# Kernel tuning notes

Measured on AMD Instinct MI355X. Metric: run time of the kernel, lower is better.

## Reference

```python
import jax, jax.numpy as jnp
import numpy as np
import math

HIDDEN = 128   # hidden_size (per-head dim) used for 1/sqrt(d) scaling
SPAN = 1024    # attn_span
B, M = 32, 1024
K_LEN = M + SPAN


def _unskew(X, span):
    """X: [B, M, K] -> [B, M, span], out[b,m,l] = X[b, m, m+l].
    Equivalent to the torch pad/view/slice trick (shift row m left by m)."""
    _, Mq, _ = X.shape
    rows = jnp.arange(Mq)[:, None]                 # [M,1]
    cols = rows + jnp.arange(span)[None, :]        # [M,span]
    return X[:, rows, cols]


def _skew(X, pad_value):
    """X: [B, M, L] -> [B, M, M+L], out[b,m,j] = X[b,m,j-m] if 0<=j-m<L else pad.
    Equivalent to the torch pad/view/slice trick (shift row m right by m)."""
    _, Mq, L = X.shape
    m = jnp.arange(Mq)[:, None]                    # [M,1]
    rel = jnp.arange(Mq + L)[None, :] - m          # [M, M+L]
    valid = (rel >= 0) & (rel < L)
    gathered = X[:, m, jnp.clip(rel, 0, L - 1)]    # [B, M, M+L]
    return jnp.where(valid, gathered, pad_value)


def setup_inputs() -> dict:
    key = jax.random.key(0)
    k1, k2, k3, k4 = jax.random.split(key, 4)
    return {
        "query": jax.random.normal(k1, (B, M, HIDDEN), dtype=jnp.float32),
        "key": jax.random.normal(k2, (B, K_LEN, HIDDEN), dtype=jnp.float32),
        "value": jax.random.normal(k3, (B, K_LEN, HIDDEN), dtype=jnp.float32),
        "pos_encoding": jax.random.normal(k4, (HIDDEN, SPAN), dtype=jnp.float32),
    }


def reference(query, key, value, pos_encoding):
    span = pos_encoding.shape[-1]
    # context scores: [B, M, M+span]
    attn_ctx = jnp.einsum('bmh,bkh->bmk', query, key)
    attn_ctx = _unskew(attn_ctx, span)             # [B, M, span]
    # relative-position scores: [B, M, span]
    attn_pos = jnp.einsum('bmh,hl->bml', query, pos_encoding)
    attn = (attn_ctx + attn_pos) / math.sqrt(HIDDEN)
    attn = jax.nn.softmax(attn, axis=-1)           # dropout p=0 -> identity
    attn_sk = _skew(attn, 0.0)                     # [B, M, M+span]
    return jnp.einsum('bmk,bkh->bmh', attn_sk, value)
```

## Files before the change

kernel.cpp:

```cpp
#include <hip/hip_runtime.h>
#include <hip/hip_bf16.h>

#define B_    32
#define M_    1024
#define H_    128
#define SPAN_ 1024
#define KL_   2048
#define NITER 17

typedef __attribute__((ext_vector_type(8))) short bf16x8;
typedef __attribute__((ext_vector_type(4))) float f32x4;

#define PITCH_A  264
#define PITCH_VT 136
#define PITCH_PR 264
#define PITCH_PW 136
#define OFF_K  0
#define OFF_VT 16896
#define OFF_PT 34304
#define OFF_PR 51200
#define OFF_PW 68096
#define LDS_TOTAL 76800
#define SCALE 0.08838834764831845f

static __device__ __forceinline__ unsigned int cvt_pk2(float lo, float hi) {
  unsigned int r;
  asm("v_cvt_pk_bf16_f32 %0, %1, %2" : "=v"(r) : "v"(lo), "v"(hi));
  return r;
}
static __device__ __forceinline__ unsigned short f2b(float x) {
  unsigned int u = __builtin_bit_cast(unsigned int, x);
  return (unsigned short)((u + 0x7FFFu + ((u >> 16) & 1u)) >> 16);
}
static __device__ __forceinline__ float b2f(unsigned short u) {
  return __builtin_bit_cast(float, ((unsigned int)u) << 16);
}
static __device__ __forceinline__ bf16x8 ldfrag(const char* p) {
  short4 a = *(const short4*)p;
  short4 b = *(const short4*)(p + 8);
  bf16x8 r;
  r[0] = a.x; r[1] = a.y; r[2] = a.z; r[3] = a.w;
  r[4] = b.x; r[5] = b.y; r[6] = b.z; r[7] = b.w;
  return r;
}

__global__ void __launch_bounds__(256, 2) seqattn_kernel(
    const float* __restrict__ q, const float* __restrict__ kkey,
    const float* __restrict__ vval, const float* __restrict__ pe,
    float* __restrict__ out) {
  extern __shared__ char smem[];
  char* KL = smem + OFF_K;
  char* VT = smem + OFF_VT;
  char* PT = smem + OFF_PT;
  char* PR = smem + OFF_PR;
  char* PW = smem + OFF_PW;

  int jb = blockIdx.x;
  int o  = (jb & 7) * 64 + (jb >> 3);
  int b  = o >> 4;
  int m0 = (o & 15) * 64;

  int tid  = threadIdx.x;
  int w    = tid >> 6;
  int lane = tid & 63;
  int g    = lane >> 4;
  int c    = lane & 15;
  int r0   = tid >> 5;
  int c4   = tid & 31;

  const float* qbase = q    + ((size_t)b * M_  + m0) * H_;
  const float* kbase = kkey + ((size_t)b * KL_ + m0) * H_;
  const float* vbase = vval + ((size_t)b * KL_ + m0) * H_;

  float4 kpre[8];
  float  vpre[32];
  float  ppre[32];

#define LOADK(tt) do {                                                        \
    const float* kb_ = kbase + (size_t)(64 * (tt)) * H_;                      \
    _Pragma("unroll")                                                         \
    for (int p = 0; p < 8; ++p)                                               \
      kpre[p] = *(const float4*)(kb_ + (p * 8 + r0) * H_ + c4 * 4);           \
  } while (0)

#define WRITEK() do {                                                         \
    _Pragma("unroll")                                                         \
    for (int p = 0; p < 8; ++p) {                                             \
      float4 v_ = kpre[p];                                                    \
      uint2 d_; d_.x = cvt_pk2(v_.x, v_.y); d_.y = cvt_pk2(v_.z, v_.w);       \
      *(uint2*)(KL + (p * 8 + r0) * PITCH_A + c4 * 8) = d_;                   \
    }                                                                         \
  } while (0)

#define LOADV(tt) do {                                                        \
    const float* vb_ = vbase + (size_t)(64 * (tt)) * H_;                      \
    _Pragma("unroll")                                                         \
    for (int qq = 0; qq < 4; ++qq) {                                          \
      int kq_ = 4 * (4 * w + qq);                                             \
      _Pragma("unroll")                                                       \
      for (int r = 0; r < 4; ++r) {                                           \
        vpre[qq * 8 + r * 2 + 0] = vb_[(kq_ + r) * H_ + lane];                \
        vpre[qq * 8 + r * 2 + 1] = vb_[(kq_ + r) * H_ + lane + 64];           \
      }                                                                       \
    }                                                                         \
  } while (0)

#define WRITEV() do {                                                         \
    _Pragma("unroll")                                                         \
    for (int qq = 0; qq < 4; ++qq) {                                          \
      int kq_ = 4 * w + qq;                                                   \
      uint2 lo_, hi_;                                                         \
      lo_.x = cvt_pk2(vpre[qq * 8 + 0], vpre[qq * 8 + 2]);                    \
      lo_.y = cvt_pk2(vpre[qq * 8 + 4], vpre[qq * 8 + 6]);                    \
      hi_.x = cvt_pk2(vpre[qq * 8 + 1], vpre[qq * 8 + 3]);                    \
      hi_.y = cvt_pk2(vpre[qq * 8 + 5], vpre[qq * 8 + 7]);                    \
      *(uint2*)(VT + lane * PITCH_VT + 8 * kq_) = lo_;                        \
      *(uint2*)(VT + (lane + 64) * PITCH_VT + 8 * kq_) = hi_;                 \
    }                                                                         \
  } while (0)

#define LOADP(tt) do {                                                        \
    const float* pb_ = pe + 64 * (tt);                                        \
    _Pragma("unroll")                                                         \
    for (int qq = 0; qq < 8; ++qq) {                                          \
      int h_ = 4 * (8 * w + qq);                                              \
      _Pragma("unroll")                                                       \
      for (int r = 0; r < 4; ++r)                                             \
        ppre[qq * 4 + r] = pb_[(h_ + r) * SPAN_ + lane];                      \
    }                                                                         \
  } while (0)

#define WRITEP() do {                                                         \
    _Pragma("unroll")                                                         \
    for (int qq = 0; qq < 8; ++qq) {                                          \
      uint2 d_;                                                               \
      d_.x = cvt_pk2(ppre[qq * 4 + 0], ppre[qq * 4 + 1]);                     \
      d_.y = cvt_pk2(ppre[qq * 4 + 2], ppre[qq * 4 + 3]);                     \
      *(uint2*)(PT + lane * PITCH_A + 8 * (8 * w + qq)) = d_;                 \
    }                                                                         \
  } while (0)

  {
    float4 qpre[8];
#pragma unroll
    for (int p = 0; p < 8; ++p)
      qpre[p] = *(const float4*)(qbase + (p * 8 + r0) * H_ + c4 * 4);
    LOADK(0); LOADV(0); LOADP(0);
#pragma unroll
    for (int p = 0; p < 8; ++p) {
      float4 v_ = qpre[p];
      uint2 d_;
      d_.x = cvt_pk2(v_.x * SCALE, v_.y * SCALE);
      d_.y = cvt_pk2(v_.z * SCALE, v_.w * SCALE);
      *(uint2*)(PR + (p * 8 + r0) * PITCH_PR + c4 * 8) = d_;
    }
    WRITEK(); WRITEV(); WRITEP();
    LOADK(1); LOADV(1); LOADP(1);
  }
  __syncthreads();

  bf16x8 qf[4];
#pragma unroll
  for (int hs = 0; hs < 4; ++hs)
    qf[hs] = ldfrag(PR + (w * 16 + c) * PITCH_PR + hs * 64 + g * 16);

  f32x4 O[8];
#pragma unroll
  for (int i = 0; i < 8; ++i) { O[i][0] = 0.f; O[i][1] = 0.f; O[i][2] = 0.f; O[i][3] = 0.f; }
  float mrun = -1e30f, lrun = 0.f;
  const int mrow = 16 * w + c;
  char* prRow = PR + mrow * PITCH_PR;
  char* pwRow = PW + mrow * PITCH_PW;

#pragma unroll 1
  for (int t = 0; t < NITER; ++t) {
    if (t < 16) {
#pragma unroll
      for (int lt = 0; lt < 4; ++lt) {
        f32x4 pb = {0.f, 0.f, 0.f, 0.f};
#pragma unroll
        for (int hs = 0; hs < 4; ++hs)
          pb = __builtin_amdgcn_mfma_f32_16x16x32_bf16(
              ldfrag(PT + (16 * lt + c) * PITCH_A + hs * 64 + g * 16), qf[hs], pb, 0, 0, 0);
#pragma unroll
        for (int rr = 0; rr < 4; ++rr) {
          int x = (64 * t + 16 * lt + 4 * g + rr + mrow) & 127;
          *(unsigned short*)(prRow + x * 2) = f2b(pb[rr]);
        }
      }
    }

    f32x4 s[4];
#pragma unroll
    for (int nt = 0; nt < 4; ++nt) {
      f32x4 acc = {0.f, 0.f, 0.f, 0.f};
#pragma unroll
      for (int hs = 0; hs < 4; ++hs)
        acc = __builtin_amdgcn_mfma_f32_16x16x32_bf16(
            ldfrag(KL + (16 * nt + c) * PITCH_A + hs * 64 + g * 16), qf[hs], acc, 0, 0, 0);
      s[nt] = acc;
    }

#pragma unroll
    for (int nt = 0; nt < 4; ++nt) {
      int x = (64 * t + 16 * nt + 4 * g) & 127;
      ushort4 bv = *(const ushort4*)(prRow + x * 2);
      int lbase = 64 * t + 16 * nt + 4 * g - mrow;
      const unsigned short* bp = (const unsigned short*)&bv;
#pragma unroll
      for (int rr = 0; rr < 4; ++rr) {
        float sv = s[nt][rr] + b2f(bp[rr]);
        s[nt][rr] = ((unsigned)(lbase + rr) < 1024u) ? sv : -1e30f;
      }
    }

    float pmax = -1e30f;
#pragma unroll
    for (int nt = 0; nt < 4; ++nt)
#pragma unroll
      for (int rr = 0; rr < 4; ++rr) pmax = fmaxf(pmax, s[nt][rr]);
    pmax = fmaxf(pmax, __shfl_xor(pmax, 16, 64));
    pmax = fmaxf(pmax, __shfl_xor(pmax, 32, 64));

    if (__any(pmax > mrun + 8.0f)) {
      float mn = fmaxf(mrun, pmax);
      float corr = __expf(mrun - mn);
      mrun = mn;
      lrun *= corr;
#pragma unroll
      for (int i = 0; i < 8; ++i) {
        O[i][0] *= corr; O[i][1] *= corr; O[i][2] *= corr; O[i][3] *= corr;
      }
    }

    float rsum = 0.f;
#pragma unroll
    for (int nt = 0; nt < 4; ++nt) {
      float p0 = __expf(s[nt][0] - mrun);
      float p1 = __expf(s[nt][1] - mrun);
      float p2 = __expf(s[nt][2] - mrun);
      float p3 = __expf(s[nt][3] - mrun);
      rsum += (p0 + p1) + (p2 + p3);
      uint2 d_;
      d_.x = cvt_pk2(p0, p1);
      d_.y = cvt_pk2(p2, p3);
      *(uint2*)(pwRow + (16 * nt + 4 * g) * 2) = d_;
    }
    rsum += __shfl_xor(rsum, 16, 64);
    rsum += __shfl_xor(rsum, 32, 64);
    lrun += rsum;

#pragma unroll
    for (int ks = 0; ks < 2; ++ks) {
      bf16x8 pfrag = ldfrag(pwRow + ks * 64 + g * 16);
#pragma unroll
      for (int nt = 0; nt < 8; ++nt)
        O[nt] = __builtin_amdgcn_mfma_f32_16x16x32_bf16(
            ldfrag(VT + (16 * nt + c) * PITCH_VT + ks * 64 + g * 16), pfrag, O[nt], 0, 0, 0);
    }

    __syncthreads();
    if (t < 16) {
      WRITEK(); WRITEV();
      if (t < 15) {
        WRITEP();
        LOADK(t + 2); LOADV(t + 2);
        if (t + 2 < 16) LOADP(t + 2);
      }
    }
    __syncthreads();
  }

  float inv = 1.0f / lrun;
  float* ob = out + ((size_t)b * M_ + m0 + mrow) * H_;
#pragma unroll
  for (int nt = 0; nt < 8; ++nt) {
    float4 vv;
    vv.x = O[nt][0] * inv; vv.y = O[nt][1] * inv;
    vv.z = O[nt][2] * inv; vv.w = O[nt][3] * inv;
    *(float4*)(ob + 16 * nt + 4 * g) = vv;
  }
}

extern "C" void kernel_launch(void* const* d_in, const int* in_sizes, int n_in,
                              void* d_out, int out_size, void* d_ws, size_t ws_size,
                              hipStream_t stream) {
  const float* q  = (const float*)d_in[0];
  const float* k  = (const float*)d_in[1];
  const float* v  = (const float*)d_in[2];
  const float* pe = (const float*)d_in[3];
  float* out = (float*)d_out;

  hipFuncSetAttribute(reinterpret_cast<const void*>(seqattn_kernel),
                      hipFuncAttributeMaxDynamicSharedMemorySize, LDS_TOTAL);
  seqattn_kernel<<<dim3(512), dim3(256), LDS_TOTAL, stream>>>(q, k, v, pe, out);
}
```

Before: 79.07 us.

## Pre-convert Q/K/V/pos to swizzled bf16 in workspace and stream via global_load_lds

Adds four pre-pass kernels that convert query (pre-scaled), key, transposed value and transposed pos_encoding to bf16 in a workspace, laid out in an XOR-swizzled tile layout. The main attention kernel then loads these tiles directly into LDS with global_load_lds, with no register staging or conversion in the loop, and hoists V fragments into registers so the next tile's prefetch can be issued earlier. This cuts fp32 global traffic and per-iteration conversion work inside the main loop. The cost is extra launches and a full extra read/write pass over the inputs. The old kernel stays as a fallback when the workspace is too small.

```diff
diff --git a/kernel.cpp b/kernel.cpp
--- a/kernel.cpp
+++ b/kernel.cpp
@@ -7,9 +7,289 @@
 #define SPAN_ 1024
 #define KL_   2048
 #define NITER 17
+#define SCALE 0.08838834764831845f
 
 typedef __attribute__((ext_vector_type(8))) short bf16x8;
 typedef __attribute__((ext_vector_type(4))) float f32x4;
+
+#define QOFF 0ull
+#define KOFF 8388608ull
+#define VOFF 25165824ull
+#define POFF 41943040ull
+#define WSNEED 42205184ull
+
+static __device__ __forceinline__ unsigned int cvt_pk2(float lo, float hi) {
+  unsigned int r;
+  asm("v_cvt_pk_bf16_f32 %0, %1, %2" : "=v"(r) : "v"(lo), "v"(hi));
+  return r;
+}
+static __device__ __forceinline__ unsigned short f2b(float x) {
+  unsigned int u = __builtin_bit_cast(unsigned int, x);
+  return (unsigned short)((u + 0x7FFFu + ((u >> 16) & 1u)) >> 16);
+}
+static __device__ __forceinline__ float b2f(unsigned short u) {
+  return __builtin_bit_cast(float, ((unsigned int)u) << 16);
+}
+static __device__ __forceinline__ bf16x8 ldfrag(const char* p) {
+  short4 a = *(const short4*)p;
+  short4 b = *(const short4*)(p + 8);
+  bf16x8 r;
+  r[0] = a.x; r[1] = a.y; r[2] = a.z; r[3] = a.w;
+  r[4] = b.x; r[5] = b.y; r[6] = b.z; r[7] = b.w;
+  return r;
+}
+static __device__ __forceinline__ void gll16(char* lds, const char* g) {
+  __builtin_amdgcn_global_load_lds(
+      (const __attribute__((address_space(1))) unsigned int*)g,
+      (__attribute__((address_space(3))) unsigned int*)lds, 16, 0, 0);
+}
+
+__global__ void convA(const float* __restrict__ in, char* __restrict__ out,
+                      int nunits, float scale) {
+  int idx = blockIdx.x * 256 + threadIdx.x;
+  if (idx >= nunits) return;
+  int r = idx >> 4, u = idx & 15;
+  const float* p = in + (size_t)r * 128 + u * 8;
+  float4 a = *(const float4*)p, b = *(const float4*)(p + 4);
+  uint4 d;
+  d.x = cvt_pk2(a.x * scale, a.y * scale);
+  d.y = cvt_pk2(a.z * scale, a.w * scale);
+  d.z = cvt_pk2(b.x * scale, b.y * scale);
+  d.w = cvt_pk2(b.z * scale, b.w * scale);
+  *(uint4*)(out + (size_t)r * 256 + 16 * (u ^ (r & 7))) = d;
+}
+
+__global__ void convV(const float* __restrict__ v, char* __restrict__ out) {
+  __shared__ float tile[64][130];
+  int tb = blockIdx.x;
+  const float* src = v + (size_t)tb * 64 * 128;
+  int tid = threadIdx.x;
+#pragma unroll
+  for (int i = 0; i < 8; ++i) {
+    int idx = i * 256 + tid;
+    int row = idx >> 5, c4 = idx & 31;
+    float4 x = *(const float4*)(src + row * 128 + c4 * 4);
+    tile[row][c4 * 4 + 0] = x.x; tile[row][c4 * 4 + 1] = x.y;
+    tile[row][c4 * 4 + 2] = x.z; tile[row][c4 * 4 + 3] = x.w;
+  }
+  __syncthreads();
+  char* dst = out + (size_t)tb * 16384;
+#pragma unroll
+  for (int j = 0; j < 4; ++j) {
+    int idx = j * 256 + tid;
+    int h = idx >> 3, u = idx & 7;
+    uint4 d;
+    d.x = cvt_pk2(tile[8 * u + 0][h], tile[8 * u + 1][h]);
+    d.y = cvt_pk2(tile[8 * u + 2][h], tile[8 * u + 3][h]);
+    d.z = cvt_pk2(tile[8 * u + 4][h], tile[8 * u + 5][h]);
+    d.w = cvt_pk2(tile[8 * u + 6][h], tile[8 * u + 7][h]);
+    *(uint4*)(dst + h * 128 + 16 * (u ^ (h & 7))) = d;
+  }
+}
+
+__global__ void convP(const float* __restrict__ pe, char* __restrict__ out) {
+  __shared__ float tile[128][66];
+  int lt = blockIdx.x, tid = threadIdx.x;
+#pragma unroll
+  for (int i = 0; i < 8; ++i) {
+    int idx = i * 256 + tid;
+    int h = idx >> 4, c4 = idx & 15;
+    float4 x = *(const float4*)(pe + (size_t)h * 1024 + lt * 64 + c4 * 4);
+    tile[h][c4 * 4 + 0] = x.x; tile[h][c4 * 4 + 1] = x.y;
+    tile[h][c4 * 4 + 2] = x.z; tile[h][c4 * 4 + 3] = x.w;
+  }
+  __syncthreads();
+  char* dst = out + (size_t)lt * 16384;
+#pragma unroll
+  for (int j = 0; j < 4; ++j) {
+    int idx = j * 256 + tid;
+    int l = idx >> 4, u = idx & 15;
+    uint4 d;
+    d.x = cvt_pk2(tile[8 * u + 0][l], tile[8 * u + 1][l]);
+    d.y = cvt_pk2(tile[8 * u + 2][l], tile[8 * u + 3][l]);
+    d.z = cvt_pk2(tile[8 * u + 4][l], tile[8 * u + 5][l]);
+    d.w = cvt_pk2(tile[8 * u + 6][l], tile[8 * u + 7][l]);
+    *(uint4*)(dst + l * 256 + 16 * (u ^ (l & 7))) = d;
+  }
+}
+
+#define L_KL 0
+#define L_VT 16384
+#define L_PT 32768
+#define L_PR 49152
+#define L_PW 66048
+#define LDS_MAIN 74752
+
+__global__ void __launch_bounds__(256, 2) seqattn_main(
+    const char* __restrict__ qws, const char* __restrict__ kws,
+    const char* __restrict__ vws, const char* __restrict__ pws,
+    float* __restrict__ out) {
+  extern __shared__ char smem[];
+  char* KL = smem + L_KL;
+  char* VT = smem + L_VT;
+  char* PT = smem + L_PT;
+  char* PR = smem + L_PR;
+  char* PW = smem + L_PW;
+
+  int jb = blockIdx.x;
+  int o  = (jb & 7) * 64 + (jb >> 3);
+  int b  = o >> 4;
+  int m0t = o & 15;
+
+  int tid = threadIdx.x, w = tid >> 6, lane = tid & 63, g = lane >> 4, c = lane & 15;
+  int mrow = 16 * w + c;
+  int sx = c & 7;
+  int foffA[4], foffV[2];
+#pragma unroll
+  for (int hs = 0; hs < 4; ++hs) foffA[hs] = 16 * (((hs << 2) | g) ^ sx);
+  foffV[0] = 16 * (g ^ sx);
+  foffV[1] = 16 * ((4 | g) ^ sx);
+
+  const char* qsrc = qws + ((size_t)(b * 16 + m0t)) * 16384;
+  const char* ksrc = kws + ((size_t)(b * 32 + m0t)) * 16384;
+  const char* vsrc = vws + ((size_t)(b * 32 + m0t)) * 16384;
+
+#pragma unroll
+  for (int i = 0; i < 4; ++i)
+    gll16(KL + (4 * w + i) * 1024, qsrc + (4 * w + i) * 1024 + lane * 16);
+  __syncthreads();
+  bf16x8 qf[4];
+#pragma unroll
+  for (int hs = 0; hs < 4; ++hs)
+    qf[hs] = *(const bf16x8*)(KL + mrow * 256 + foffA[hs]);
+  __syncthreads();
+#pragma unroll
+  for (int i = 0; i < 4; ++i) {
+    gll16(KL + (4 * w + i) * 1024, ksrc + (4 * w + i) * 1024 + lane * 16);
+    gll16(VT + (4 * w + i) * 1024, vsrc + (4 * w + i) * 1024 + lane * 16);
+    gll16(PT + (4 * w + i) * 1024, pws + (4 * w + i) * 1024 + lane * 16);
+  }
+  __syncthreads();
+
+  f32x4 O[8];
+#pragma unroll
+  for (int i = 0; i < 8; ++i) { O[i][0] = 0.f; O[i][1] = 0.f; O[i][2] = 0.f; O[i][3] = 0.f; }
+  float mrun = -1e30f, lrun = 0.f;
+  char* prRow = PR + mrow * 264;
+  char* pwRow = PW + mrow * 136;
+
+#pragma unroll 1
+  for (int t = 0; t < NITER; ++t) {
+    if (t < 16) {
+#pragma unroll
+      for (int lt = 0; lt < 4; ++lt) {
+        f32x4 pb = {0.f, 0.f, 0.f, 0.f};
+#pragma unroll
+        for (int hs = 0; hs < 4; ++hs)
+          pb = __builtin_amdgcn_mfma_f32_16x16x32_bf16(
+              *(const bf16x8*)(PT + (16 * lt + c) * 256 + foffA[hs]), qf[hs], pb, 0, 0, 0);
+#pragma unroll
+        for (int rr = 0; rr < 4; ++rr) {
+          int x = (64 * t + 16 * lt + 4 * g + rr + mrow) & 127;
+          *(unsigned short*)(prRow + x * 2) = f2b(pb[rr]);
+        }
+      }
+    }
+    f32x4 s[4];
+#pragma unroll
+    for (int nt = 0; nt < 4; ++nt) {
+      f32x4 acc = {0.f, 0.f, 0.f, 0.f};
+#pragma unroll
+      for (int hs = 0; hs < 4; ++hs)
+        acc = __builtin_amdgcn_mfma_f32_16x16x32_bf16(
+            *(const bf16x8*)(KL + (16 * nt + c) * 256 + foffA[hs]), qf[hs], acc, 0, 0, 0);
+      s[nt] = acc;
+    }
+    bf16x8 vf[16];
+#pragma unroll
+    for (int nt = 0; nt < 8; ++nt)
+#pragma unroll
+      for (int ks = 0; ks < 2; ++ks)
+        vf[nt * 2 + ks] = *(const bf16x8*)(VT + (16 * nt + c) * 128 + foffV[ks]);
+
+    __syncthreads();
+    if (t < 16) {
+      const char* ks_ = ksrc + (size_t)(t + 1) * 16384;
+      const char* vs_ = vsrc + (size_t)(t + 1) * 16384;
+#pragma unroll
+      for (int i = 0; i < 4; ++i) {
+        gll16(KL + (4 * w + i) * 1024, ks_ + (4 * w + i) * 1024 + lane * 16);
+        gll16(VT + (4 * w + i) * 1024, vs_ + (4 * w + i) * 1024 + lane * 16);
+      }
+      if (t < 15) {
+        const char* ps_ = pws + (size_t)(t + 1) * 16384;
+#pragma unroll
+        for (int i = 0; i < 4; ++i)
+          gll16(PT + (4 * w + i) * 1024, ps_ + (4 * w + i) * 1024 + lane * 16);
+      }
+    }
+
+#pragma unroll
+    for (int nt = 0; nt < 4; ++nt) {
+      int x = (64 * t + 16 * nt + 4 * g) & 127;
+      ushort4 bv = *(const ushort4*)(prRow + x * 2);
+      int lbase = 64 * t + 16 * nt + 4 * g - mrow;
+      const unsigned short* bp = (const unsigned short*)&bv;
+#pragma unroll
+      for (int rr = 0; rr < 4; ++rr) {
+        float sv = s[nt][rr] + b2f(bp[rr]);
+        s[nt][rr] = ((unsigned)(lbase + rr) < 1024u) ? sv : -1e30f;
+      }
+    }
+    float pmax = -1e30f;
+#pragma unroll
+    for (int nt = 0; nt < 4; ++nt)
+#pragma unroll
+      for (int rr = 0; rr < 4; ++rr) pmax = fmaxf(pmax, s[nt][rr]);
+    pmax = fmaxf(pmax, __shfl_xor(pmax, 16, 64));
+    pmax = fmaxf(pmax, __shfl_xor(pmax, 32, 64));
+    if (__any(pmax > mrun + 8.0f)) {
+      float mn = fmaxf(mrun, pmax);
+      float corr = __expf(mrun - mn);
+      mrun = mn;
+      lrun *= corr;
+#pragma unroll
+      for (int i = 0; i < 8; ++i) {
+        O[i][0] *= corr; O[i][1] *= corr; O[i][2] *= corr; O[i][3] *= corr;
+      }
+    }
+    float rsum = 0.f;
+#pragma unroll
+    for (int nt = 0; nt < 4; ++nt) {
+      float p0 = __expf(s[nt][0] - mrun);
+      float p1 = __expf(s[nt][1] - mrun);
+      float p2 = __expf(s[nt][2] - mrun);
+      float p3 = __expf(s[nt][3] - mrun);
+      rsum += (p0 + p1) + (p2 + p3);
+      uint2 d_;
+      d_.x = cvt_pk2(p0, p1);
+      d_.y = cvt_pk2(p2, p3);
+      *(uint2*)(pwRow + (16 * nt + 4 * g) * 2) = d_;
+    }
+    rsum += __shfl_xor(rsum, 16, 64);
+    rsum += __shfl_xor(rsum, 32, 64);
+    lrun += rsum;
+#pragma unroll
+    for (int ks = 0; ks < 2; ++ks) {
+      bf16x8 pfrag = ldfrag(pwRow + ks * 64 + g * 16);
+#pragma unroll
+      for (int nt = 0; nt < 8; ++nt)
+        O[nt] = __builtin_amdgcn_mfma_f32_16x16x32_bf16(
+            vf[nt * 2 + ks], pfrag, O[nt], 0, 0, 0);
+    }
+    __syncthreads();
+  }
+
+  float inv = 1.0f / lrun;
+  float* ob = out + ((size_t)b * M_ + m0t * 64 + mrow) * H_;
+#pragma unroll
+  for (int nt = 0; nt < 8; ++nt) {
+    float4 vv;
+    vv.x = O[nt][0] * inv; vv.y = O[nt][1] * inv;
+    vv.z = O[nt][2] * inv; vv.w = O[nt][3] * inv;
+    *(float4*)(ob + 16 * nt + 4 * g) = vv;
+  }
+}
 
 #define PITCH_A  264
 #define PITCH_VT 136
@@ -20,31 +300,9 @@
 #define OFF_PT 34304
 #define OFF_PR 51200
 #define OFF_PW 68096
-#define LDS_TOTAL 76800
-#define SCALE 0.08838834764831845f
-
-static __device__ __forceinline__ unsigned int cvt_pk2(float lo, float hi) {
-  unsigned int r;
-  asm("v_cvt_pk_bf16_f32 %0, %1, %2" : "=v"(r) : "v"(lo), "v"(hi));
-  return r;
-}
-static __device__ __forceinline__ unsigned short f2b(float x) {
-  unsigned int u = __builtin_bit_cast(unsigned int, x);
-  return (unsigned short)((u + 0x7FFFu + ((u >> 16) & 1u)) >> 16);
-}
-static __device__ __forceinline__ float b2f(unsigned short u) {
-  return __builtin_bit_cast(float, ((unsigned int)u) << 16);
-}
-static __device__ __forceinline__ bf16x8 ldfrag(const char* p) {
-  short4 a = *(const short4*)p;
-  short4 b = *(const short4*)(p + 8);
-  bf16x8 r;
-  r[0] = a.x; r[1] = a.y; r[2] = a.z; r[3] = a.w;
-  r[4] = b.x; r[5] = b.y; r[6] = b.z; r[7] = b.w;
-  return r;
-}
-
-__global__ void __launch_bounds__(256, 2) seqattn_kernel(
+#define LDS_FB 76800
+
+__global__ void __launch_bounds__(256, 2) seqattn_fb(
     const float* __restrict__ q, const float* __restrict__ kkey,
     const float* __restrict__ vval, const float* __restrict__ pe,
     float* __restrict__ out) {
@@ -82,7 +340,6 @@
     for (int p = 0; p < 8; ++p)                                               \
       kpre[p] = *(const float4*)(kb_ + (p * 8 + r0) * H_ + c4 * 4);           \
   } while (0)
-
 #define WRITEK() do {                                                         \
     _Pragma("unroll")                                                         \
     for (int p = 0; p < 8; ++p) {                                             \
@@ -91,7 +348,6 @@
       *(uint2*)(KL + (p * 8 + r0) * PITCH_A + c4 * 8) = d_;                   \
     }                                                                         \
   } while (0)
-
 #define LOADV(tt) do {                                                        \
     const float* vb_ = vbase + (size_t)(64 * (tt)) * H_;                      \
     _Pragma("unroll")                                                         \
@@ -104,7 +360,6 @@
       }                                                                       \
     }                                                                         \
   } while (0)
-
 #define WRITEV() do {                                                         \
     _Pragma("unroll")                                                         \
     for (int qq = 0; qq < 4; ++qq) {                                          \
@@ -118,7 +373,6 @@
       *(uint2*)(VT + (lane + 64) * PITCH_VT + 8 * kq_) = hi_;                 \
     }                                                                         \
   } while (0)
-
 #define LOADP(tt) do {                                                        \
     const float* pb_ = pe + 64 * (tt);                                        \
     _Pragma("unroll")                                                         \
@@ -129,7 +383,6 @@
         ppre[qq * 4 + r] = pb_[(h_ + r) * SPAN_ + lane];                      \
     }                                                                         \
   } while (0)
-
 #define WRITEP() do {                                                         \
     _Pragma("unroll")                                                         \
     for (int qq = 0; qq < 8; ++qq) {                                          \
@@ -189,7 +442,6 @@
         }
       }
     }
-
     f32x4 s[4];
 #pragma unroll
     for (int nt = 0; nt < 4; ++nt) {
@@ -200,7 +452,6 @@
             ldfrag(KL + (16 * nt + c) * PITCH_A + hs * 64 + g * 16), qf[hs], acc, 0, 0, 0);
       s[nt] = acc;
     }
-
 #pragma unroll
     for (int nt = 0; nt < 4; ++nt) {
       int x = (64 * t + 16 * nt + 4 * g) & 127;
@@ -213,7 +464,6 @@
         s[nt][rr] = ((unsigned)(lbase + rr) < 1024u) ? sv : -1e30f;
       }
     }
-
     float pmax = -1e30f;
 #pragma unroll
     for (int nt = 0; nt < 4; ++nt)
@@ -221,7 +471,6 @@
       for (int rr = 0; rr < 4; ++rr) pmax = fmaxf(pmax, s[nt][rr]);
     pmax = fmaxf(pmax, __shfl_xor(pmax, 16, 64));
     pmax = fmaxf(pmax, __shfl_xor(pmax, 32, 64));
-
     if (__any(pmax > mrun + 8.0f)) {
       float mn = fmaxf(mrun, pmax);
       float corr = __expf(mrun - mn);
@@ -232,7 +481,6 @@
         O[i][0] *= corr; O[i][1] *= corr; O[i][2] *= corr; O[i][3] *= corr;
       }
     }
-
     float rsum = 0.f;
 #pragma unroll
     for (int nt = 0; nt < 4; ++nt) {
@@ -249,7 +497,6 @@
     rsum += __shfl_xor(rsum, 16, 64);
     rsum += __shfl_xor(rsum, 32, 64);
     lrun += rsum;
-
 #pragma unroll
     for (int ks = 0; ks < 2; ++ks) {
       bf16x8 pfrag = ldfrag(pwRow + ks * 64 + g * 16);
@@ -258,7 +505,6 @@
         O[nt] = __builtin_amdgcn_mfma_f32_16x16x32_bf16(
             ldfrag(VT + (16 * nt + c) * PITCH_VT + ks * 64 + g * 16), pfrag, O[nt], 0, 0, 0);
     }
-
     __syncthreads();
     if (t < 16) {
       WRITEK(); WRITEV();
@@ -281,6 +527,12 @@
     *(float4*)(ob + 16 * nt + 4 * g) = vv;
   }
 }
+#undef LOADK
+#undef WRITEK
+#undef LOADV
+#undef WRITEV
+#undef LOADP
+#undef WRITEP
 
 extern "C" void kernel_launch(void* const* d_in, const int* in_sizes, int n_in,
                               void* d_out, int out_size, void* d_ws, size_t ws_size,
@@ -291,7 +543,19 @@
   const float* pe = (const float*)d_in[3];
   float* out = (float*)d_out;
 
-  hipFuncSetAttribute(reinterpret_cast<const void*>(seqattn_kernel),
-                      hipFuncAttributeMaxDynamicSharedMemorySize, LDS_TOTAL);
-  seqattn_kernel<<<dim3(512), dim3(256), LDS_TOTAL, stream>>>(q, k, v, pe, out);
-}
+  if (ws_size >= WSNEED) {
+    char* ws = (char*)d_ws;
+    convA<<<dim3(2048), dim3(256), 0, stream>>>(q, ws + QOFF, 32 * 1024 * 16, SCALE);
+    convA<<<dim3(4096), dim3(256), 0, stream>>>(k, ws + KOFF, 32 * 2048 * 16, 1.0f);
+    convV<<<dim3(1024), dim3(256), 0, stream>>>(v, ws + VOFF);
+    convP<<<dim3(16), dim3(256), 0, stream>>>(pe, ws + POFF);
+    hipFuncSetAttribute(reinterpret_cast<const void*>(seqattn_main),
+                        hipFuncAttributeMaxDynamicSharedMemorySize, LDS_MAIN);
+    seqattn_main<<<dim3(512), dim3(256), LDS_MAIN, stream>>>(
+        ws + QOFF, ws + KOFF, ws + VOFF, ws + POFF, out);
+  } else {
+    hipFuncSetAttribute(reinterpret_cast<const void*>(seqattn_fb),
+                        hipFuncAttributeMaxDynamicSharedMemorySize, LDS_FB);
+    seqattn_fb<<<dim3(512), dim3(256), LDS_FB, stream>>>(q, k, v, pe, out);
+  }
+}
```

After: 88.43 us. +11.8%, slower.

## Precompute bf16 transposed pos-encoding in workspace and restructure main loop pipeline

Applied to the files above, without the earlier changes.

Adds a small pre-kernel that converts the positional encoding to bf16 in a fragment-friendly transposed layout inside the workspace. The main kernel then reads position fragments straight from global/L2 and no longer stages them through LDS, which shrinks LDS use and the per-tile prefetch registers. The loop is reordered to write K/V into LDS first, sync, then issue the next tile's global loads before the MFMAs. It also uses wider float2 V loads, 16-byte fragment LDS reads with new pitches, and s_setprio around the MFMA blocks. The old kernel remains as a fallback when the workspace is too small, at the cost of an extra launch and an additional barrier per iteration.

```diff
diff --git a/kernel.cpp b/kernel.cpp
--- a/kernel.cpp
+++ b/kernel.cpp
@@ -7,21 +7,12 @@
 #define SPAN_ 1024
 #define KL_   2048
 #define NITER 17
+#define SCALE 0.08838834764831845f
 
 typedef __attribute__((ext_vector_type(8))) short bf16x8;
 typedef __attribute__((ext_vector_type(4))) float f32x4;
 
-#define PITCH_A  264
-#define PITCH_VT 136
-#define PITCH_PR 264
-#define PITCH_PW 136
-#define OFF_K  0
-#define OFF_VT 16896
-#define OFF_PT 34304
-#define OFF_PR 51200
-#define OFF_PW 68096
-#define LDS_TOTAL 76800
-#define SCALE 0.08838834764831845f
+#define WSNEED 262144ull
 
 static __device__ __forceinline__ unsigned int cvt_pk2(float lo, float hi) {
   unsigned int r;
@@ -44,16 +35,51 @@
   return r;
 }
 
-__global__ void __launch_bounds__(256, 2) seqattn_kernel(
+__global__ void __launch_bounds__(256) convP2(const float* __restrict__ pe,
+                                              char* __restrict__ out) {
+  __shared__ float tile[128 * 66];
+  int lt = blockIdx.x, tid = threadIdx.x;
+#pragma unroll
+  for (int i = 0; i < 8; ++i) {
+    int idx = i * 256 + tid;
+    int h = idx >> 4, c4 = idx & 15;
+    float4 x = *(const float4*)(pe + (size_t)h * 1024 + lt * 64 + c4 * 4);
+    tile[h * 66 + c4 * 4 + 0] = x.x; tile[h * 66 + c4 * 4 + 1] = x.y;
+    tile[h * 66 + c4 * 4 + 2] = x.z; tile[h * 66 + c4 * 4 + 3] = x.w;
+  }
+  __syncthreads();
+  char* dst = out + (size_t)lt * 16384;
+#pragma unroll
+  for (int j = 0; j < 4; ++j) {
+    int u = tid >> 4;
+    int l = (tid & 15) + 16 * j;
+    uint4 d;
+    d.x = cvt_pk2(tile[(8 * u + 0) * 66 + l], tile[(8 * u + 1) * 66 + l]);
+    d.y = cvt_pk2(tile[(8 * u + 2) * 66 + l], tile[(8 * u + 3) * 66 + l]);
+    d.z = cvt_pk2(tile[(8 * u + 4) * 66 + l], tile[(8 * u + 5) * 66 + l]);
+    d.w = cvt_pk2(tile[(8 * u + 6) * 66 + l], tile[(8 * u + 7) * 66 + l]);
+    *(uint4*)(dst + l * 256 + 16 * u) = d;
+  }
+}
+
+#define MP_A  272
+#define MP_V  144
+#define MP_W  144
+#define L_KL  0
+#define L_VT  17408
+#define L_PR  35840
+#define L_PW  53248
+#define LDS_MAIN 62464
+
+__global__ void __launch_bounds__(256, 2) seqattn_main(
     const float* __restrict__ q, const float* __restrict__ kkey,
-    const float* __restrict__ vval, const float* __restrict__ pe,
+    const float* __restrict__ vval, const char* __restrict__ posws,
     float* __restrict__ out) {
   extern __shared__ char smem[];
-  char* KL = smem + OFF_K;
-  char* VT = smem + OFF_VT;
-  char* PT = smem + OFF_PT;
-  char* PR = smem + OFF_PR;
-  char* PW = smem + OFF_PW;
+  char* KLp = smem + L_KL;
+  char* VTp = smem + L_VT;
+  char* PRp = smem + L_PR;
+  char* PWp = smem + L_PW;
 
   int jb = blockIdx.x;
   int o  = (jb & 7) * 64 + (jb >> 3);
@@ -67,76 +93,53 @@
   int c    = lane & 15;
   int r0   = tid >> 5;
   int c4   = tid & 31;
+  int mrow = 16 * w + c;
 
   const float* qbase = q    + ((size_t)b * M_  + m0) * H_;
   const float* kbase = kkey + ((size_t)b * KL_ + m0) * H_;
   const float* vbase = vval + ((size_t)b * KL_ + m0) * H_;
 
   float4 kpre[8];
-  float  vpre[32];
-  float  ppre[32];
-
-#define LOADK(tt) do {                                                        \
+  float2 vpre[16];
+
+#define MLOADK(tt) do {                                                       \
     const float* kb_ = kbase + (size_t)(64 * (tt)) * H_;                      \
     _Pragma("unroll")                                                         \
     for (int p = 0; p < 8; ++p)                                               \
       kpre[p] = *(const float4*)(kb_ + (p * 8 + r0) * H_ + c4 * 4);           \
   } while (0)
 
-#define WRITEK() do {                                                         \
+#define MWRITEK() do {                                                        \
     _Pragma("unroll")                                                         \
     for (int p = 0; p < 8; ++p) {                                             \
       float4 v_ = kpre[p];                                                    \
       uint2 d_; d_.x = cvt_pk2(v_.x, v_.y); d_.y = cvt_pk2(v_.z, v_.w);       \
-      *(uint2*)(KL + (p * 8 + r0) * PITCH_A + c4 * 8) = d_;                   \
-    }                                                                         \
-  } while (0)
-
-#define LOADV(tt) do {                                                        \
+      *(uint2*)(KLp + (p * 8 + r0) * MP_A + c4 * 8) = d_;                     \
+    }                                                                         \
+  } while (0)
+
+#define MLOADV(tt) do {                                                       \
     const float* vb_ = vbase + (size_t)(64 * (tt)) * H_;                      \
     _Pragma("unroll")                                                         \
     for (int qq = 0; qq < 4; ++qq) {                                          \
       int kq_ = 4 * (4 * w + qq);                                             \
       _Pragma("unroll")                                                       \
-      for (int r = 0; r < 4; ++r) {                                           \
-        vpre[qq * 8 + r * 2 + 0] = vb_[(kq_ + r) * H_ + lane];                \
-        vpre[qq * 8 + r * 2 + 1] = vb_[(kq_ + r) * H_ + lane + 64];           \
-      }                                                                       \
-    }                                                                         \
-  } while (0)
-
-#define WRITEV() do {                                                         \
+      for (int r = 0; r < 4; ++r)                                             \
+        vpre[qq * 4 + r] = *(const float2*)(vb_ + (kq_ + r) * H_ + 2 * lane); \
+    }                                                                         \
+  } while (0)
+
+#define MWRITEV() do {                                                        \
     _Pragma("unroll")                                                         \
     for (int qq = 0; qq < 4; ++qq) {                                          \
       int kq_ = 4 * w + qq;                                                   \
       uint2 lo_, hi_;                                                         \
-      lo_.x = cvt_pk2(vpre[qq * 8 + 0], vpre[qq * 8 + 2]);                    \
-      lo_.y = cvt_pk2(vpre[qq * 8 + 4], vpre[qq * 8 + 6]);                    \
-      hi_.x = cvt_pk2(vpre[qq * 8 + 1], vpre[qq * 8 + 3]);                    \
-      hi_.y = cvt_pk2(vpre[qq * 8 + 5], vpre[qq * 8 + 7]);                    \
-      *(uint2*)(VT + lane * PITCH_VT + 8 * kq_) = lo_;                        \
-      *(uint2*)(VT + (lane + 64) * PITCH_VT + 8 * kq_) = hi_;                 \
-    }                                                                         \
-  } while (0)
-
-#define LOADP(tt) do {                                                        \
-    const float* pb_ = pe + 64 * (tt);                                        \
-    _Pragma("unroll")                                                         \
-    for (int qq = 0; qq < 8; ++qq) {                                          \
-      int h_ = 4 * (8 * w + qq);                                              \
-      _Pragma("unroll")                                                       \
-      for (int r = 0; r < 4; ++r)                                             \
-        ppre[qq * 4 + r] = pb_[(h_ + r) * SPAN_ + lane];                      \
-    }                                                                         \
-  } while (0)
-
-#define WRITEP() do {                                                         \
-    _Pragma("unroll")                                                         \
-    for (int qq = 0; qq < 8; ++qq) {                                          \
-      uint2 d_;                                                               \
-      d_.x = cvt_pk2(ppre[qq * 4 + 0], ppre[qq * 4 + 1]);                     \
-      d_.y = cvt_pk2(ppre[qq * 4 + 2], ppre[qq * 4 + 3]);                     \
-      *(uint2*)(PT + lane * PITCH_A + 8 * (8 * w + qq)) = d_;                 \
+      lo_.x = cvt_pk2(vpre[qq * 4 + 0].x, vpre[qq * 4 + 1].x);                \
+      lo_.y = cvt_pk2(vpre[qq * 4 + 2].x, vpre[qq * 4 + 3].x);                \
+      hi_.x = cvt_pk2(vpre[qq * 4 + 0].y, vpre[qq * 4 + 1].y);                \
+      hi_.y = cvt_pk2(vpre[qq * 4 + 2].y, vpre[qq * 4 + 3].y);                \
+      *(uint2*)(VTp + (2 * lane + 0) * MP_V + 8 * kq_) = lo_;                 \
+      *(uint2*)(VTp + (2 * lane + 1) * MP_V + 8 * kq_) = hi_;                 \
     }                                                                         \
   } while (0)
 
@@ -145,66 +148,79 @@
 #pragma unroll
     for (int p = 0; p < 8; ++p)
       qpre[p] = *(const float4*)(qbase + (p * 8 + r0) * H_ + c4 * 4);
-    LOADK(0); LOADV(0); LOADP(0);
+    MLOADK(0); MLOADV(0);
 #pragma unroll
     for (int p = 0; p < 8; ++p) {
       float4 v_ = qpre[p];
       uint2 d_;
       d_.x = cvt_pk2(v_.x * SCALE, v_.y * SCALE);
       d_.y = cvt_pk2(v_.z * SCALE, v_.w * SCALE);
-      *(uint2*)(PR + (p * 8 + r0) * PITCH_PR + c4 * 8) = d_;
-    }
-    WRITEK(); WRITEV(); WRITEP();
-    LOADK(1); LOADV(1); LOADP(1);
+      *(uint2*)(PRp + (p * 8 + r0) * MP_A + c4 * 8) = d_;
+    }
   }
   __syncthreads();
 
   bf16x8 qf[4];
 #pragma unroll
   for (int hs = 0; hs < 4; ++hs)
-    qf[hs] = ldfrag(PR + (w * 16 + c) * PITCH_PR + hs * 64 + g * 16);
+    qf[hs] = *(const bf16x8*)(PRp + mrow * MP_A + hs * 64 + g * 16);
+  __syncthreads();
 
   f32x4 O[8];
 #pragma unroll
   for (int i = 0; i < 8; ++i) { O[i][0] = 0.f; O[i][1] = 0.f; O[i][2] = 0.f; O[i][3] = 0.f; }
   float mrun = -1e30f, lrun = 0.f;
-  const int mrow = 16 * w + c;
-  char* prRow = PR + mrow * PITCH_PR;
-  char* pwRow = PW + mrow * PITCH_PW;
+  char* prRow = PRp + mrow * MP_A;
+  char* pwRow = PWp + mrow * MP_W;
 
 #pragma unroll 1
   for (int t = 0; t < NITER; ++t) {
+    MWRITEK();
+    MWRITEV();
+
     if (t < 16) {
+      const char* pt = posws + (size_t)t * 16384;
+      int xbase = (64 * t + mrow) & 127;
 #pragma unroll
       for (int lt = 0; lt < 4; ++lt) {
         f32x4 pb = {0.f, 0.f, 0.f, 0.f};
 #pragma unroll
-        for (int hs = 0; hs < 4; ++hs)
-          pb = __builtin_amdgcn_mfma_f32_16x16x32_bf16(
-              ldfrag(PT + (16 * lt + c) * PITCH_A + hs * 64 + g * 16), qf[hs], pb, 0, 0, 0);
+        for (int hs = 0; hs < 4; ++hs) {
+          bf16x8 pf = *(const bf16x8*)(pt + (16 * lt + c) * 256 + hs * 64 + g * 16);
+          pb = __builtin_amdgcn_mfma_f32_16x16x32_bf16(pf, qf[hs], pb, 0, 0, 0);
+        }
+        int xb = xbase + 16 * lt + 4 * g;
 #pragma unroll
         for (int rr = 0; rr < 4; ++rr) {
-          int x = (64 * t + 16 * lt + 4 * g + rr + mrow) & 127;
+          int x = xb + rr;
+          x = (x >= 128) ? x - 128 : x;
           *(unsigned short*)(prRow + x * 2) = f2b(pb[rr]);
         }
       }
     }
+    __syncthreads();
+
+    if (t < 16) { MLOADK(t + 1); MLOADV(t + 1); }
+    __builtin_amdgcn_sched_barrier(0);
 
     f32x4 s[4];
+    __builtin_amdgcn_s_setprio(1);
 #pragma unroll
     for (int nt = 0; nt < 4; ++nt) {
       f32x4 acc = {0.f, 0.f, 0.f, 0.f};
 #pragma unroll
-      for (int hs = 0; hs < 4; ++hs)
-        acc = __builtin_amdgcn_mfma_f32_16x16x32_bf16(
-            ldfrag(KL + (16 * nt + c) * PITCH_A + hs * 64 + g * 16), qf[hs], acc, 0, 0, 0);
+      for (int hs = 0; hs < 4; ++hs) {
+        bf16x8 kf = *(const bf16x8*)(KLp + (16 * nt + c) * MP_A + hs * 64 + g * 16);
+        acc = __builtin_amdgcn_mfma_f32_16x16x32_bf16(kf, qf[hs], acc, 0, 0, 0);
+      }
       s[nt] = acc;
     }
+    __builtin_amdgcn_s_setprio(0);
 
 #pragma unroll
     for (int nt = 0; nt < 4; ++nt) {
-      int x = (64 * t + 16 * nt + 4 * g) & 127;
-      ushort4 bv = *(const ushort4*)(prRow + x * 2);
+      int x4 = (64 * t + 16 * nt + 4 * g) & 127;
+      ushort4 bv = *(const ushort4*)(prRow + x4 * 2);
       int lbase = 64 * t + 16 * nt + 4 * g - mrow;
       const unsigned short* bp = (const unsigned short*)&bv;
 #pragma unroll
@@ -221,7 +237,6 @@
       for (int rr = 0; rr < 4; ++rr) pmax = fmaxf(pmax, s[nt][rr]);
     pmax = fmaxf(pmax, __shfl_xor(pmax, 16, 64));
     pmax = fmaxf(pmax, __shfl_xor(pmax, 32, 64));
-
     if (__any(pmax > mrun + 8.0f)) {
       float mn = fmaxf(mrun, pmax);
       float corr = __expf(mrun - mn);
@@ -232,7 +247,6 @@
         O[i][0] *= corr; O[i][1] *= corr; O[i][2] *= corr; O[i][3] *= corr;
       }
     }
-
     float rsum = 0.f;
 #pragma unroll
     for (int nt = 0; nt < 4; ++nt) {
@@ -250,6 +264,237 @@
     rsum += __shfl_xor(rsum, 32, 64);
     lrun += rsum;
 
+    __builtin_amdgcn_s_setprio(1);
+#pragma unroll
+    for (int ks = 0; ks < 2; ++ks) {
+      bf16x8 pfrag = *(const bf16x8*)(pwRow + ks * 64 + g * 16);
+#pragma unroll
+      for (int nt = 0; nt < 8; ++nt) {
+        bf16x8 vfr = *(const bf16x8*)(VTp + (16 * nt + c) * MP_V + ks * 64 + g * 16);
+        O[nt] = __builtin_amdgcn_mfma_f32_16x16x32_bf16(vfr, pfrag, O[nt], 0, 0, 0);
+      }
+    }
+    __builtin_amdgcn_s_setprio(0);
+    __syncthreads();
+  }
+
+  float inv = 1.0f / lrun;
+  float* ob = out + ((size_t)b * M_ + m0 + mrow) * H_;
+#pragma unroll
+  for (int nt = 0; nt < 8; ++nt) {
+    float4 vv;
+    vv.x = O[nt][0] * inv; vv.y = O[nt][1] * inv;
+    vv.z = O[nt][2] * inv; vv.w = O[nt][3] * inv;
+    *(float4*)(ob + 16 * nt + 4 * g) = vv;
+  }
+}
+
+#define PITCH_A  264
+#define PITCH_VT 136
+#define PITCH_PR 264
+#define PITCH_PW 136
+#define OFF_K  0
+#define OFF_VT 16896
+#define OFF_PT 34304
+#define OFF_PR 51200
+#define OFF_PW 68096
+#define LDS_FB 76800
+
+__global__ void __launch_bounds__(256, 2) seqattn_fb(
+    const float* __restrict__ q, const float* __restrict__ kkey,
+    const float* __restrict__ vval, const float* __restrict__ pe,
+    float* __restrict__ out) {
+  extern __shared__ char smem[];
+  char* KL = smem + OFF_K;
+  char* VT = smem + OFF_VT;
+  char* PT = smem + OFF_PT;
+  char* PR = smem + OFF_PR;
+  char* PW = smem + OFF_PW;
+
+  int jb = blockIdx.x;
+  int o  = (jb & 7) * 64 + (jb >> 3);
+  int b  = o >> 4;
+  int m0 = (o & 15) * 64;
+
+  int tid  = threadIdx.x;
+  int w    = tid >> 6;
+  int lane = tid & 63;
+  int g    = lane >> 4;
+  int c    = lane & 15;
+  int r0   = tid >> 5;
+  int c4   = tid & 31;
+
+  const float* qbase = q    + ((size_t)b * M_  + m0) * H_;
+  const float* kbase = kkey + ((size_t)b * KL_ + m0) * H_;
+  const float* vbase = vval + ((size_t)b * KL_ + m0) * H_;
+
+  float4 kpre[8];
+  float  vpre[32];
+  float  ppre[32];
+
+#define LOADK(tt) do {                                                        \
+    const float* kb_ = kbase + (size_t)(64 * (tt)) * H_;                      \
+    _Pragma("unroll")                                                         \
+    for (int p = 0; p < 8; ++p)                                               \
+      kpre[p] = *(const float4*)(kb_ + (p * 8 + r0) * H_ + c4 * 4);           \
+  } while (0)
+#define WRITEK() do {                                                         \
+    _Pragma("unroll")                                                         \
+    for (int p = 0; p < 8; ++p) {                                             \
+      float4 v_ = kpre[p];                                                    \
+      uint2 d_; d_.x = cvt_pk2(v_.x, v_.y); d_.y = cvt_pk2(v_.z, v_.w);       \
+      *(uint2*)(KL + (p * 8 + r0) * PITCH_A + c4 * 8) = d_;                   \
+    }                                                                         \
+  } while (0)
+#define LOADV(tt) do {                                                        \
+    const float* vb_ = vbase + (size_t)(64 * (tt)) * H_;                      \
+    _Pragma("unroll")                                                         \
+    for (int qq = 0; qq < 4; ++qq) {                                          \
+      int kq_ = 4 * (4 * w + qq);                                             \
+      _Pragma("unroll")                                                       \
+      for (int r = 0; r < 4; ++r) {                                           \
+        vpre[qq * 8 + r * 2 + 0] = vb_[(kq_ + r) * H_ + lane];                \
+        vpre[qq * 8 + r * 2 + 1] = vb_[(kq_ + r) * H_ + lane + 64];           \
+      }                                                                       \
+    }                                                                         \
+  } while (0)
+#define WRITEV() do {                                                         \
+    _Pragma("unroll")                                                         \
+    for (int qq = 0; qq < 4; ++qq) {                                          \
+      int kq_ = 4 * w + qq;                                                   \
+      uint2 lo_, hi_;                                                         \
+      lo_.x = cvt_pk2(vpre[qq * 8 + 0], vpre[qq * 8 + 2]);                    \
+      lo_.y = cvt_pk2(vpre[qq * 8 + 4], vpre[qq * 8 + 6]);                    \
+      hi_.x = cvt_pk2(vpre[qq * 8 + 1], vpre[qq * 8 + 3]);                    \
+      hi_.y = cvt_pk2(vpre[qq * 8 + 5], vpre[qq * 8 + 7]);                    \
+      *(uint2*)(VT + lane * PITCH_VT + 8 * kq_) = lo_;                        \
+      *(uint2*)(VT + (lane + 64) * PITCH_VT + 8 * kq_) = hi_;                 \
+    }                                                                         \
+  } while (0)
+#define LOADP(tt) do {                                                        \
+    const float* pb_ = pe + 64 * (tt);                                        \
+    _Pragma("unroll")                                                         \
+    for (int qq = 0; qq < 8; ++qq) {                                          \
+      int h_ = 4 * (8 * w + qq);                                              \
+      _Pragma("unroll")                                                       \
+      for (int r = 0; r < 4; ++r)                                             \
+        ppre[qq * 4 + r] = pb_[(h_ + r) * SPAN_ + lane];                      \
+    }                                                                         \
+  } while (0)
+#define WRITEP() do {                                                         \
+    _Pragma("unroll")                                                         \
+    for (int qq = 0; qq < 8; ++qq) {                                          \
+      uint2 d_;                                                               \
+      d_.x = cvt_pk2(ppre[qq * 4 + 0], ppre[qq * 4 + 1]);                     \
+      d_.y = cvt_pk2(ppre[qq * 4 + 2], ppre[qq * 4 + 3]);                     \
+      *(uint2*)(PT + lane * PITCH_A + 8 * (8 * w + qq)) = d_;                 \
+    }                                                                         \
+  } while (0)
+
+  {
+    float4 qpre[8];
+#pragma unroll
+    for (int p = 0; p < 8; ++p)
+      qpre[p] = *(const float4*)(qbase + (p * 8 + r0) * H_ + c4 * 4);
+    LOADK(0); LOADV(0); LOADP(0);
+#pragma unroll
+    for (int p = 0; p < 8; ++p) {
+      float4 v_ = qpre[p];
+      uint2 d_;
+      d_.x = cvt_pk2(v_.x * SCALE, v_.y * SCALE);
+      d_.y = cvt_pk2(v_.z * SCALE, v_.w * SCALE);
+      *(uint2*)(PR + (p * 8 + r0) * PITCH_PR + c4 * 8) = d_;
+    }
+    WRITEK(); WRITEV(); WRITEP();
+    LOADK(1); LOADV(1); LOADP(1);
+  }
+  __syncthreads();
+
+  bf16x8 qf[4];
+#pragma unroll
+  for (int hs = 0; hs < 4; ++hs)
+    qf[hs] = ldfrag(PR + (w * 16 + c) * PITCH_PR + hs * 64 + g * 16);
+
+  f32x4 O[8];
+#pragma unroll
+  for (int i = 0; i < 8; ++i) { O[i][0] = 0.f; O[i][1] = 0.f; O[i][2] = 0.f; O[i][3] = 0.f; }
+  float mrun = -1e30f, lrun = 0.f;
+  const int mrow = 16 * w + c;
+  char* prRow = PR + mrow * PITCH_PR;
+  char* pwRow = PW + mrow * PITCH_PW;
+
+#pragma unroll 1
+  for (int t = 0; t < NITER; ++t) {
+    if (t < 16) {
+#pragma unroll
+      for (int lt = 0; lt < 4; ++lt) {
+        f32x4 pb = {0.f, 0.f, 0.f, 0.f};
+#pragma unroll
+        for (int hs = 0; hs < 4; ++hs)
+          pb = __builtin_amdgcn_mfma_f32_16x16x32_bf16(
+              ldfrag(PT + (16 * lt + c) * PITCH_A + hs * 64 + g * 16), qf[hs], pb, 0, 0, 0);
+#pragma unroll
+        for (int rr = 0; rr < 4; ++rr) {
+          int x = (64 * t + 16 * lt + 4 * g + rr + mrow) & 127;
+          *(unsigned short*)(prRow + x * 2) = f2b(pb[rr]);
+        }
+      }
+    }
+    f32x4 s[4];
+#pragma unroll
+    for (int nt = 0; nt < 4; ++nt) {
+      f32x4 acc = {0.f, 0.f, 0.f, 0.f};
+#pragma unroll
+      for (int hs = 0; hs < 4; ++hs)
+        acc = __builtin_amdgcn_mfma_f32_16x16x32_bf16(
+            ldfrag(KL + (16 * nt + c) * PITCH_A + hs * 64 + g * 16), qf[hs], acc, 0, 0, 0);
+      s[nt] = acc;
+    }
+#pragma unroll
+    for (int nt = 0; nt < 4; ++nt) {
+      int x = (64 * t + 16 * nt + 4 * g) & 127;
+      ushort4 bv = *(const ushort4*)(prRow + x * 2);
+      int lbase = 64 * t + 16 * nt + 4 * g - mrow;
+      const unsigned short* bp = (const unsigned short*)&bv;
+#pragma unroll
+      for (int rr = 0; rr < 4; ++rr) {
+        float sv = s[nt][rr] + b2f(bp[rr]);
+        s[nt][rr] = ((unsigned)(lbase + rr) < 1024u) ? sv : -1e30f;
+      }
+    }
+    float pmax = -1e30f;
+#pragma unroll
+    for (int nt = 0; nt < 4; ++nt)
+#pragma unroll
+      for (int rr = 0; rr < 4; ++rr) pmax = fmaxf(pmax, s[nt][rr]);
+    pmax = fmaxf(pmax, __shfl_xor(pmax, 16, 64));
+    pmax = fmaxf(pmax, __shfl_xor(pmax, 32, 64));
+    if (__any(pmax > mrun + 8.0f)) {
+      float mn = fmaxf(mrun, pmax);
+      float corr = __expf(mrun - mn);
+      mrun = mn;
+      lrun *= corr;
+#pragma unroll
+      for (int i = 0; i < 8; ++i) {
+        O[i][0] *= corr; O[i][1] *= corr; O[i][2] *= corr; O[i][3] *= corr;
+      }
+    }
+    float rsum = 0.f;
+#pragma unroll
+    for (int nt = 0; nt < 4; ++nt) {
+      float p0 = __expf(s[nt][0] - mrun);
+      float p1 = __expf(s[nt][1] - mrun);
+      float p2 = __expf(s[nt][2] - mrun);
+      float p3 = __expf(s[nt][3] - mrun);
+      rsum += (p0 + p1) + (p2 + p3);
+      uint2 d_;
+      d_.x = cvt_pk2(p0, p1);
+      d_.y = cvt_pk2(p2, p3);
+      *(uint2*)(pwRow + (16 * nt + 4 * g) * 2) = d_;
+    }
+    rsum += __shfl_xor(rsum, 16, 64);
+    rsum += __shfl_xor(rsum, 32, 64);
+    lrun += rsum;
 #pragma unroll
     for (int ks = 0; ks < 2; ++ks) {
       bf16x8 pfrag = ldfrag(pwRow + ks * 64 + g * 16);
@@ -258,7 +503,6 @@
         O[nt] = __builtin_amdgcn_mfma_f32_16x16x32_bf16(
             ldfrag(VT + (16 * nt + c) * PITCH_VT + ks * 64 + g * 16), pfrag, O[nt], 0, 0, 0);
     }
-
     __syncthreads();
     if (t < 16) {
       WRITEK(); WRITEV();
@@ -281,6 +525,12 @@
     *(float4*)(ob + 16 * nt + 4 * g) = vv;
   }
 }
+#undef LOADK
+#undef WRITEK
+#undef LOADV
+#undef WRITEV
+#undef LOADP
+#undef WRITEP
 
 extern "C" void kernel_launch(void* const* d_in, const int* in_sizes, int n_in,
                               void* d_out, int out_size, void* d_ws, size_t ws_size,
@@ -291,7 +541,13 @@
   const float* pe = (const float*)d_in[3];
   float* out = (float*)d_out;
 
-  hipFuncSetAttribute(reinterpret_cast<const void*>(seqattn_kernel),
-                      hipFuncAttributeMaxDynamicSharedMemorySize, LDS_TOTAL);
-  seqattn_kernel<<<dim3(512), dim3(256), LDS_TOTAL, stream>>>(q, k, v, pe, out);
-}
+  if (ws_size >= WSNEED) {
+    char* ws = (char*)d_ws;
+    convP2<<<dim3(16), dim3(256), 0, stream>>>(pe, ws);
+    seqattn_main<<<dim3(512), dim3(256), LDS_MAIN, stream>>>(q, k, v, ws, out);
+  } else {
+    (void)hipFuncSetAttribute(reinterpret_cast<const void*>(seqattn_fb),
+                              hipFuncAttributeMaxDynamicSharedMemorySize, LDS_FB);
+    seqattn_fb<<<dim3(512), dim3(256), LDS_FB, stream>>>(q, k, v, pe, out);
+  }
+}
```

Measured after the change: 112.9 us. +42.8%, slower.
